# Optimization experiments

Measured on AMD Instinct MI355X. Metric: run time of the kernel, lower is better.

The kernel has to match this reference:

```python
import jax, jax.numpy as jnp
import numpy as np

T = 100  # number of time steps
B = 256
F = 4096

def setup_inputs() -> dict:
    key = jax.random.key(0)
    k1, k2 = jax.random.split(key)
    x = jax.random.uniform(k1, (B, F), dtype=jnp.float32)
    delays = jax.random.uniform(k2, (F,), dtype=jnp.float32)
    return {"x": x, "delays": delays}

def reference(x, delays):
    # spike_times: [B, F] int, truncation toward zero like torch .long()
    st = ((1.0 - x * delays[None, :]) * (T - 1)).astype(jnp.int32)
    st = jnp.clip(st, 0, T - 1)
    # one-hot over time axis -> [B, T, F]
    t_axis = jnp.arange(T, dtype=jnp.int32)[None, :, None]  # [1, T, 1]
    spikes = (t_axis == st[:, None, :]).astype(jnp.float32)
    return spikes
```

## Files before the change

kernel.cpp:

```cpp
#include <hip/hip_runtime.h>

constexpr int T  = 100;
constexpr int B  = 256;
constexpr int F  = 4096;
constexpr int F4 = F / 4;

typedef float        floatx4 __attribute__((ext_vector_type(4)));
typedef unsigned int u32;

__global__ __launch_bounds__(256) void build_st(
    const float* __restrict__ x,
    const float* __restrict__ delays,
    u32* __restrict__ stw)
{
    const int idx = blockIdx.x * 256 + threadIdx.x;
    const int f4  = idx & (F4 - 1);

    const floatx4 xv = reinterpret_cast<const floatx4*>(x)[idx];
    const floatx4 dv = reinterpret_cast<const floatx4*>(delays)[f4];

    auto sti = [](float xi, float di) -> u32 {
        float p  = __fmul_rn(xi, di);
        float s  = __fsub_rn(1.0f, p);
        float v  = __fmul_rn(s, 99.0f);
        int   st = (int)v;
        st = st < 0 ? 0 : st;
        st = st > (T - 1) ? (T - 1) : st;
        return (u32)st;
    };

    const u32 w = sti(xv.x, dv.x)
                | (sti(xv.y, dv.y) << 8)
                | (sti(xv.z, dv.z) << 16)
                | (sti(xv.w, dv.w) << 24);
    stw[idx] = w;
}

constexpr int BLOCK  = 256;
constexpr int NBLK   = 2048;
constexpr int G      = NBLK * BLOCK;
constexpr int TOTAL4 = B * T * F4;
constexpr int NITER  = TOTAL4 / G;

__global__ __launch_bounds__(BLOCK) void write_spikes(
    const u32* __restrict__ stw,
    float* __restrict__ out)
{
    const int tid0 = blockIdx.x * BLOCK + threadIdx.x;
    const int f4   = tid0 & (F4 - 1);
    floatx4* out4  = reinterpret_cast<floatx4*>(out);

    int idx = tid0;
    for (int k = 0; k < NITER; ++k, idx += G) {
        const int bt = idx >> 10;
        const int b  = (bt * 5243) >> 19;
        const int t  = bt - b * 100;

        const u32 w = stw[(b << 10) | f4];

        floatx4 v;
        v.x = (t == (int)( w        & 255u)) ? 1.0f : 0.0f;
        v.y = (t == (int)((w >> 8)  & 255u)) ? 1.0f : 0.0f;
        v.z = (t == (int)((w >> 16) & 255u)) ? 1.0f : 0.0f;
        v.w = (t == (int)( w >> 24        )) ? 1.0f : 0.0f;

        out4[idx] = v;
    }
}

__global__ __launch_bounds__(256) void spike_kernel_fb(
    const float* __restrict__ x,
    const float* __restrict__ delays,
    float* __restrict__ out)
{
    const int idx = blockIdx.x * blockDim.x + threadIdx.x;
    const int f4  = idx & (F4 - 1);
    const int b   = idx >> 10;

    const floatx4 xv = reinterpret_cast<const floatx4*>(x)[idx];
    const floatx4 dv = reinterpret_cast<const floatx4*>(delays)[f4];

    auto spike_time = [](float xi, float di) -> int {
        float p  = __fmul_rn(xi, di);
        float s  = __fsub_rn(1.0f, p);
        float v  = __fmul_rn(s, 99.0f);
        int   st = (int)v;
        st = st < 0 ? 0 : st;
        st = st > (T - 1) ? (T - 1) : st;
        return st;
    };
    const int st0 = spike_time(xv.x, dv.x);
    const int st1 = spike_time(xv.y, dv.y);
    const int st2 = spike_time(xv.z, dv.z);
    const int st3 = spike_time(xv.w, dv.w);

    floatx4* outp = reinterpret_cast<floatx4*>(out) + (size_t)b * T * F4 + f4;
#pragma unroll 4
    for (int t = 0; t < T; ++t) {
        floatx4 v;
        v.x = (t == st0) ? 1.0f : 0.0f;
        v.y = (t == st1) ? 1.0f : 0.0f;
        v.z = (t == st2) ? 1.0f : 0.0f;
        v.w = (t == st3) ? 1.0f : 0.0f;
        outp[(size_t)t * F4] = v;
    }
}

extern "C" void kernel_launch(void* const* d_in, const int* in_sizes, int n_in,
                              void* d_out, int out_size, void* d_ws, size_t ws_size,
                              hipStream_t stream)
{
    const float* x      = reinterpret_cast<const float*>(d_in[0]);
    const float* delays = reinterpret_cast<const float*>(d_in[1]);
    float* out          = reinterpret_cast<float*>(d_out);

    const size_t needed = (size_t)B * F4 * sizeof(u32);
    if (ws_size >= needed && d_ws != nullptr) {
        u32* stw = reinterpret_cast<u32*>(d_ws);
        build_st<<<B * F4 / 256, 256, 0, stream>>>(x, delays, stw);
        write_spikes<<<NBLK, BLOCK, 0, stream>>>(stw, out);
    } else {
        spike_kernel_fb<<<B * F4 / 256, 256, 0, stream>>>(x, delays, out);
    }
}
```

Baseline: 403.5 us.

## Replace dense one-hot writes with memset plus scatter of ones

The dense pass that computed and wrote every element of the B×T×F one-hot tensor is replaced. The output is now zeroed with hipMemsetAsync, and a per-(b, f4) kernel writes a single 1.0f at each spike time. This removes the per-element compare-and-select work and uses the runtime's fill path for the bulk zero traffic. The trade-off is an extra launch and scalar, uncoalesced scattered stores across different time rows. It also assumes out_size is a byte count.

```diff
diff --git a/kernel.cpp b/kernel.cpp
--- a/kernel.cpp
+++ b/kernel.cpp
@@ -36,36 +36,21 @@
     stw[idx] = w;
 }
 
-constexpr int BLOCK  = 256;
-constexpr int NBLK   = 2048;
-constexpr int G      = NBLK * BLOCK;
-constexpr int TOTAL4 = B * T * F4;
-constexpr int NITER  = TOTAL4 / G;
-
-__global__ __launch_bounds__(BLOCK) void write_spikes(
+__global__ __launch_bounds__(256) void scatter_ones(
     const u32* __restrict__ stw,
     float* __restrict__ out)
 {
-    const int tid0 = blockIdx.x * BLOCK + threadIdx.x;
-    const int f4   = tid0 & (F4 - 1);
-    floatx4* out4  = reinterpret_cast<floatx4*>(out);
+    const int idx = blockIdx.x * 256 + threadIdx.x;
+    const int f4  = idx & (F4 - 1);
+    const int b   = idx >> 10;
 
-    int idx = tid0;
-    for (int k = 0; k < NITER; ++k, idx += G) {
-        const int bt = idx >> 10;
-        const int b  = (bt * 5243) >> 19;
-        const int t  = bt - b * 100;
+    const u32 w = stw[idx];
 
-        const u32 w = stw[(b << 10) | f4];
-
-        floatx4 v;
-        v.x = (t == (int)( w        & 255u)) ? 1.0f : 0.0f;
-        v.y = (t == (int)((w >> 8)  & 255u)) ? 1.0f : 0.0f;
-        v.z = (t == (int)((w >> 16) & 255u)) ? 1.0f : 0.0f;
-        v.w = (t == (int)( w >> 24        )) ? 1.0f : 0.0f;
-
-        out4[idx] = v;
-    }
+    float* base = out + (size_t)b * T * F + (f4 << 2);
+    base[(size_t)( w         & 255u) * F + 0] = 1.0f;
+    base[(size_t)((w >> 8)   & 255u) * F + 1] = 1.0f;
+    base[(size_t)((w >> 16)  & 255u) * F + 2] = 1.0f;
+    base[(size_t)( w >> 24         ) * F + 3] = 1.0f;
 }
 
 __global__ __launch_bounds__(256) void spike_kernel_fb(
@@ -118,7 +103,8 @@
     if (ws_size >= needed && d_ws != nullptr) {
         u32* stw = reinterpret_cast<u32*>(d_ws);
         build_st<<<B * F4 / 256, 256, 0, stream>>>(x, delays, stw);
-        write_spikes<<<NBLK, BLOCK, 0, stream>>>(stw, out);
+        hipMemsetAsync(out, 0, (size_t)out_size, stream);
+        scatter_ones<<<B * F4 / 256, 256, 0, stream>>>(stw, out);
     } else {
         spike_kernel_fb<<<B * F4 / 256, 256, 0, stream>>>(x, delays, out);
     }
```

Result: slower. 420.0 us (+4.1%).
